# Kernel optimization log

Hardware: AMD Instinct MI355X
Metric: run time of the kernel (lower is better)

## Reference

```python
import jax, jax.numpy as jnp
from jax import lax
import numpy as np

B, C, H, W = 16, 64, 256, 256
K = 4


def setup_inputs() -> dict:
    key = jax.random.key(0)
    k1, k2, k3, k4 = jax.random.split(key, 4)
    x = jax.random.normal(k1, (B, C, H, W), dtype=jnp.float32)
    weight = jax.random.normal(k2, (K, C, 3, 3), dtype=jnp.float32)
    # attn 1x1 conv: weight [K, C] (squeezed 1x1 spatial), bias [K]
    attn_w = jax.random.normal(k3, (K, C), dtype=jnp.float32) * (1.0 / np.sqrt(C))
    attn_b = jax.random.normal(k4, (K,), dtype=jnp.float32) * 0.01
    return {"x": x, "weight": weight, "attn_w": attn_w, "attn_b": attn_b}


def reference(x, weight, attn_w, attn_b):
    # 1x1 conv -> logits [B, K, H, W], then softmax over the K kernels
    logits = jnp.einsum("bchw,kc->bkhw", x, attn_w) + attn_b[None, :, None, None]
    attn = jax.nn.softmax(logits, axis=1)
    # One grouped call producing all K single-channel conv outputs: [B, K, H, W]
    conv = lax.conv_general_dilated(
        x, weight,
        window_strides=(1, 1), padding="SAME",
        dimension_numbers=("NCHW", "OIHW", "NCHW"),
    )
    # attention-weighted mixture, summed over kernels -> [B, 1, H, W]
    return jnp.sum(conv * attn, axis=1, keepdims=True)
```

## Files before the change

### kernel.cpp

```cpp
#include <hip/hip_runtime.h>


typedef _Float16 half2_t __attribute__((ext_vector_type(2)));
typedef unsigned int uint;

#define HH 256
#define WW 256
#define CH 64
#define PLANE (HH * WW)
#define TILE 32
#define NG 32
#define ROWS 34
#define NC4 10
#define LDSS 41
#define BUF_DW (ROWS * LDSS)
#define TU (ROWS * NC4)
#define NS 2

#define WPK_N 1152
#define APK_OFF 1152

__device__ __forceinline__ uint pkrtz(float a, float b) {
    return __builtin_bit_cast(uint, __builtin_amdgcn_cvt_pkrtz(a, b));
}

__device__ __forceinline__ float dot2(uint a, uint b, float c) {
#if __has_builtin(__builtin_amdgcn_fdot2)
    return __builtin_amdgcn_fdot2(__builtin_bit_cast(half2_t, a),
                                  __builtin_bit_cast(half2_t, b), c, false);
#else
    half2_t ha = __builtin_bit_cast(half2_t, a);
    half2_t hb = __builtin_bit_cast(half2_t, b);
    return c + (float)ha[0] * (float)hb[0] + (float)ha[1] * (float)hb[1];
#endif
}

__global__ void kwdc_pack(const float* __restrict__ weight,
                          const float* __restrict__ attn_w,
                          uint* __restrict__ wsu) {
    int e = blockIdx.x * 256 + threadIdx.x;
    if (e < WPK_N) {
        int k = e / 288, rem = e % 288, pair = rem / 9, tap = rem % 9;
        int c0 = 2 * pair;
        wsu[e] = pkrtz(weight[(k * CH + c0) * 9 + tap],
                       weight[(k * CH + c0 + 1) * 9 + tap]);
    } else if (e < WPK_N + 128) {
        int e2 = e - WPK_N;
        int k = e2 / 32, pair = e2 % 32;
        int c0 = 2 * pair;
        wsu[APK_OFF + e2] = pkrtz(attn_w[k * CH + c0], attn_w[k * CH + c0 + 1]);
    }
}

__global__ __launch_bounds__(256, 4) void kwdc_main(
    const float* __restrict__ x,
    const uint*  __restrict__ wsu,
    const float* __restrict__ attn_b,
    float* __restrict__ out)
{
    __shared__ uint lds[2][BUF_DW];

    const int tid = threadIdx.x;

    const int fid = blockIdx.x;
    const int tw = (fid >> 3) & 7;
    const int th = fid & 7;
    const int b  = fid >> 6;

    const int r  = tid >> 3;
    const int cg = tid & 7;
    const int wb = cg * 4;

    const int h0 = th * TILE;
    const int w0 = tw * TILE;

    const float* xb = x + (size_t)b * CH * PLANE;

    int  s_gofs[NS];
    int  s_lofs[NS];
    bool s_val[NS];
    bool s_act[NS];
#pragma unroll
    for (int s = 0; s < NS; ++s) {
        int i = tid + s * 256;
        bool act = i < TU;
        int col4 = i % NC4;
        int row  = i / NC4;
        int gh  = h0 + row - 1;
        int gw0 = w0 - 4 + col4 * 4;
        s_act[s]  = act;
        s_val[s]  = act && ((unsigned)gh < HH) && ((unsigned)gw0 < WW);
        s_gofs[s] = gh * WW + gw0;
        s_lofs[s] = row * LDSS + col4 * 4;
    }

    struct Unit { float4 a, b; };
    Unit stgA[NS], stgB[NS];

    auto load_set = [&](int g, Unit* stg) {
#pragma unroll
        for (int s = 0; s < NS; ++s) {
            float4 va = {0.f, 0.f, 0.f, 0.f}, vb = va;
            if (s_val[s]) {
                const float* pa = xb + (size_t)(2 * g) * PLANE + s_gofs[s];
                va = *reinterpret_cast<const float4*>(pa);
                vb = *reinterpret_cast<const float4*>(pa + PLANE);
            }
            stg[s].a = va; stg[s].b = vb;
        }
    };

    auto store_set = [&](const Unit* stg, int buf) {
#pragma unroll
        for (int s = 0; s < NS; ++s) {
            if (s_act[s]) {
                uint* q = &lds[buf][s_lofs[s]];
                q[0] = pkrtz(stg[s].a.x, stg[s].b.x);
                q[1] = pkrtz(stg[s].a.y, stg[s].b.y);
                q[2] = pkrtz(stg[s].a.z, stg[s].b.z);
                q[3] = pkrtz(stg[s].a.w, stg[s].b.w);
            }
        }
    };

    float conv[4][4];
    float logit[4][4];
#pragma unroll
    for (int k = 0; k < 4; ++k)
#pragma unroll
        for (int p = 0; p < 4; ++p) { conv[k][p] = 0.f; logit[k][p] = 0.f; }

    load_set(0, stgA);
    store_set(stgA, 0);
    load_set(1, stgA);
    load_set(2, stgB);
    __syncthreads();

    for (int g = 0; g < NG; ++g) {
        if (g + 1 < NG) {
            Unit* setp = (g & 1) ? stgB : stgA;
            store_set(setp, (g + 1) & 1);
            if (g + 3 < NG) load_set(g + 3, setp);
        }

        uint w2[4][9];
        uint a2[4];
#pragma unroll
        for (int k = 0; k < 4; ++k) {
            const uint* wq = wsu + k * 288 + g * 9;
#pragma unroll
            for (int t = 0; t < 9; ++t) w2[k][t] = wq[t];
            a2[k] = wsu[APK_OFF + k * 32 + g];
        }

        const uint* tp = &lds[g & 1][r * LDSS + wb + 3];
        uint rv[3][6];
#pragma unroll
        for (int i = 0; i < 3; ++i)
#pragma unroll
            for (int j = 0; j < 6; ++j)
                rv[i][j] = tp[i * LDSS + j];

#pragma unroll
        for (int k = 0; k < 4; ++k) {
#pragma unroll
            for (int p = 0; p < 4; ++p) {
                float acc = conv[k][p];
                acc = dot2(rv[0][p],     w2[k][0], acc);
                acc = dot2(rv[0][p + 1], w2[k][1], acc);
                acc = dot2(rv[0][p + 2], w2[k][2], acc);
                acc = dot2(rv[1][p],     w2[k][3], acc);
                acc = dot2(rv[1][p + 1], w2[k][4], acc);
                acc = dot2(rv[1][p + 2], w2[k][5], acc);
                acc = dot2(rv[2][p],     w2[k][6], acc);
                acc = dot2(rv[2][p + 1], w2[k][7], acc);
                acc = dot2(rv[2][p + 2], w2[k][8], acc);
                conv[k][p] = acc;
                logit[k][p] = dot2(rv[1][p + 1], a2[k], logit[k][p]);
            }
        }
        __syncthreads();
    }

    const float b0 = attn_b[0], b1 = attn_b[1], b2 = attn_b[2], b3 = attn_b[3];
    float4 o;
    float* op = &o.x;
#pragma unroll
    for (int p = 0; p < 4; ++p) {
        float l0 = logit[0][p] + b0;
        float l1 = logit[1][p] + b1;
        float l2 = logit[2][p] + b2;
        float l3 = logit[3][p] + b3;
        float m = fmaxf(fmaxf(l0, l1), fmaxf(l2, l3));
        float e0 = __expf(l0 - m), e1 = __expf(l1 - m);
        float e2 = __expf(l2 - m), e3 = __expf(l3 - m);
        float s = e0 + e1 + e2 + e3;
        float num = conv[0][p] * e0 + conv[1][p] * e1
                  + conv[2][p] * e2 + conv[3][p] * e3;
        op[p] = num / s;
    }
    size_t oidx = (size_t)b * PLANE + (size_t)(h0 + r) * WW + (w0 + wb);
    *reinterpret_cast<float4*>(out + oidx) = o;
}

extern "C" void kernel_launch(void* const* d_in, const int* in_sizes, int n_in,
                              void* d_out, int out_size, void* d_ws, size_t ws_size,
                              hipStream_t stream) {
    const float* x      = (const float*)d_in[0];
    const float* weight = (const float*)d_in[1];
    const float* attn_w = (const float*)d_in[2];
    const float* attn_b = (const float*)d_in[3];
    float* out = (float*)d_out;
    uint*  wsu = (uint*)d_ws;

    kwdc_pack<<<dim3(5), 256, 0, stream>>>(weight, attn_w, wsu);
    kwdc_main<<<dim3(1024), 256, 0, stream>>>(x, wsu, attn_b, out);
}
```

Baseline: 82.25 us.

## Use single-wavefront 8-row tiles with one LDS buffer and no barriers

The kernel moves from 256-thread blocks covering 32x32 tiles with a double-buffered LDS ring and per-channel-pair __syncthreads to 64-thread single-wavefront blocks covering 8x32 tiles. Each block uses one LDS buffer. It reads the stencil rows into registers before overwriting the buffer with the next channel pair, relying on in-order LDS access within a wavefront instead of barriers. This removes barrier stalls, raises the block count for scheduling, and halves LDS use per block. The cost is that halo rows are a larger share of the tile, so more redundant global loads are issued.

```diff
diff --git a/kernel.cpp b/kernel.cpp
--- a/kernel.cpp
+++ b/kernel.cpp
@@ -8,13 +8,12 @@
 #define WW 256
 #define CH 64
 #define PLANE (HH * WW)
-#define TILE 32
 #define NG 32
-#define ROWS 34
+#define BROWS 8
+#define RROWS 10
 #define NC4 10
-#define LDSS 41
-#define BUF_DW (ROWS * LDSS)
-#define TU (ROWS * NC4)
+#define LDSS 45
+#define TU (RROWS * NC4)
 #define NS 2
 
 #define WPK_N 1152
@@ -52,27 +51,28 @@
     }
 }
 
-__global__ __launch_bounds__(256, 4) void kwdc_main(
+__global__ __launch_bounds__(64, 4) void kwdc_main(
     const float* __restrict__ x,
     const uint*  __restrict__ wsu,
     const float* __restrict__ attn_b,
     float* __restrict__ out)
 {
-    __shared__ uint lds[2][BUF_DW];
-
-    const int tid = threadIdx.x;
+    __shared__ uint lds[RROWS * LDSS];
+
+    const int lane = threadIdx.x;
 
     const int fid = blockIdx.x;
-    const int tw = (fid >> 3) & 7;
-    const int th = fid & 7;
-    const int b  = fid >> 6;
-
-    const int r  = tid >> 3;
-    const int cg = tid & 7;
+    const int tw  = fid >> 9;
+    const int rem = fid & 511;
+    const int b   = rem >> 5;
+    const int br  = rem & 31;
+
+    const int h0 = br * BROWS;
+    const int w0 = tw * 32;
+
+    const int r  = lane >> 3;
+    const int cg = lane & 7;
     const int wb = cg * 4;
-
-    const int h0 = th * TILE;
-    const int w0 = tw * TILE;
 
     const float* xb = x + (size_t)b * CH * PLANE;
 
@@ -82,7 +82,7 @@
     bool s_act[NS];
 #pragma unroll
     for (int s = 0; s < NS; ++s) {
-        int i = tid + s * 256;
+        int i = lane + s * 64;
         bool act = i < TU;
         int col4 = i % NC4;
         int row  = i / NC4;
@@ -110,11 +110,11 @@
         }
     };
 
-    auto store_set = [&](const Unit* stg, int buf) {
+    auto store_set = [&](const Unit* stg) {
 #pragma unroll
         for (int s = 0; s < NS; ++s) {
             if (s_act[s]) {
-                uint* q = &lds[buf][s_lofs[s]];
+                uint* q = &lds[s_lofs[s]];
                 q[0] = pkrtz(stg[s].a.x, stg[s].b.x);
                 q[1] = pkrtz(stg[s].a.y, stg[s].b.y);
                 q[2] = pkrtz(stg[s].a.z, stg[s].b.z);
@@ -131,15 +131,22 @@
         for (int p = 0; p < 4; ++p) { conv[k][p] = 0.f; logit[k][p] = 0.f; }
 
     load_set(0, stgA);
-    store_set(stgA, 0);
+    store_set(stgA);
     load_set(1, stgA);
     load_set(2, stgB);
-    __syncthreads();
 
     for (int g = 0; g < NG; ++g) {
+        const uint* tp = &lds[r * LDSS + wb + 3];
+        uint rv[3][6];
+#pragma unroll
+        for (int i = 0; i < 3; ++i)
+#pragma unroll
+            for (int j = 0; j < 6; ++j)
+                rv[i][j] = tp[i * LDSS + j];
+
         if (g + 1 < NG) {
             Unit* setp = (g & 1) ? stgB : stgA;
-            store_set(setp, (g + 1) & 1);
+            store_set(setp);
             if (g + 3 < NG) load_set(g + 3, setp);
         }
 
@@ -152,14 +159,6 @@
             for (int t = 0; t < 9; ++t) w2[k][t] = wq[t];
             a2[k] = wsu[APK_OFF + k * 32 + g];
         }
-
-        const uint* tp = &lds[g & 1][r * LDSS + wb + 3];
-        uint rv[3][6];
-#pragma unroll
-        for (int i = 0; i < 3; ++i)
-#pragma unroll
-            for (int j = 0; j < 6; ++j)
-                rv[i][j] = tp[i * LDSS + j];
 
 #pragma unroll
         for (int k = 0; k < 4; ++k) {
@@ -179,7 +178,6 @@
                 logit[k][p] = dot2(rv[1][p + 1], a2[k], logit[k][p]);
             }
         }
-        __syncthreads();
     }
 
     const float b0 = attn_b[0], b1 = attn_b[1], b2 = attn_b[2], b3 = attn_b[3];
@@ -214,5 +212,5 @@
     uint*  wsu = (uint*)d_ws;
 
     kwdc_pack<<<dim3(5), 256, 0, stream>>>(weight, attn_w, wsu);
-    kwdc_main<<<dim3(1024), 256, 0, stream>>>(x, wsu, attn_b, out);
-}
+    kwdc_main<<<dim3(4096), 64, 0, stream>>>(x, wsu, attn_b, out);
+}
```

Result: slower. 93.21 us (+13.3%).
